# Optimization experiments

Measured on AMD Instinct MI355X. Metric: run time of the kernel, lower is better.

Reference implementation:

```python
import jax, jax.numpy as jnp
import numpy as np

DIST_THRESH = 0.5   # stands in for config.dist_thresh
ALPHA = 0.2         # LeakyReLU negative slope
NEG_INF = -9e15     # mask value used by the original module


def setup_inputs() -> dict:
    key = jax.random.key(0)
    k1, k2, k3 = jax.random.split(key, 3)
    N, dim = 8192, 128
    nodes = jax.random.normal(k1, (N, dim), dtype=jnp.float32)
    dist = jax.random.uniform(k2, (N, N), dtype=jnp.float32)
    # xavier_uniform on (2*dim, 1) with gain 1.414
    limit = 1.414 * np.sqrt(6.0 / (2 * dim + 1))
    a = jax.random.uniform(k3, (2 * dim, 1), dtype=jnp.float32,
                           minval=-limit, maxval=limit)
    return {"nodes": nodes, "dist": dist, "a": a}


def reference(nodes, dist, a):
    # Original math: e_ij = leakyrelu([h_i || h_j] @ a). Since a = [a1; a2],
    # this equals leakyrelu(h_i @ a1 + h_j @ a2) — same values, no N^2*2dim tensor.
    dim = nodes.shape[1]
    a1 = a[:dim, 0]                      # [dim]
    a2 = a[dim:, 0]                      # [dim]
    s1 = nodes @ a1                      # [N] — contribution of row node i
    s2 = nodes @ a2                      # [N] — contribution of col node j
    e = jax.nn.leaky_relu(s1[:, None] + s2[None, :], negative_slope=ALPHA)  # [N, N]
    masked = jnp.where(dist < DIST_THRESH, e, NEG_INF)
    attention = jax.nn.softmax(masked, axis=1)   # [N, N]
    h_prime = attention @ nodes                  # [N, dim]
    return h_prime
```

## Files before the change

kernel.cpp:

```cpp
#include <hip/hip_runtime.h>
#include <stdint.h>

#define NN 8192
#define DIM 128
#define ALPHA 0.2f
#define MTILE 32
#define BTHREADS 512
#define BK 256
#define NCHUNK (NN / BK)
#define WSTRIDE (BK + 8)

typedef float f32x16 __attribute__((ext_vector_type(16)));
typedef short bf16x8 __attribute__((ext_vector_type(8)));

__device__ __forceinline__ float b2f(uint32_t u){
  uint32_t x = u << 16;
  float f;
  __builtin_memcpy(&f, &x, 4);
  return f;
}
__device__ __forceinline__ uint16_t f2b(float f){
  uint32_t x;
  __builtin_memcpy(&x, &f, 4);
  x += 0x7FFFu + ((x >> 16) & 1u);
  return (uint16_t)(x >> 16);
}

__global__ void s_kernel(const float* __restrict__ nodes,
                         const float* __restrict__ a,
                         float* __restrict__ s1, float* __restrict__ s2){
  int row  = blockIdx.x * 4 + (threadIdx.x >> 6);
  int lane = threadIdx.x & 63;
  float2 nv  = *(const float2*)(nodes + row * DIM + lane * 2);
  float2 a1v = *(const float2*)(a + lane * 2);
  float2 a2v = *(const float2*)(a + DIM + lane * 2);
  float p1 = nv.x * a1v.x + nv.y * a1v.y;
  float p2 = nv.x * a2v.x + nv.y * a2v.y;
  #pragma unroll
  for (int off = 32; off; off >>= 1){
    p1 += __shfl_down(p1, off);
    p2 += __shfl_down(p2, off);
  }
  if (lane == 0){ s1[row] = p1; s2[row] = p2; }
}

__global__ void t_kernel(const float* __restrict__ nodes,
                         uint16_t* __restrict__ nodesT){
  __shared__ uint16_t tile[32][33];
  int kb = blockIdx.x * 32, nb = blockIdx.y * 32;
  int tx = threadIdx.x & 31, ty = threadIdx.x >> 5;
  for (int r = ty; r < 32; r += 8)
    tile[r][tx] = f2b(nodes[(size_t)(kb + r) * DIM + nb + tx]);
  __syncthreads();
  for (int r = ty; r < 32; r += 8)
    nodesT[(size_t)(nb + r) * NN + kb + tx] = tile[tx][r];
}

__global__ void __launch_bounds__(BTHREADS)
attn_kernel(const float* __restrict__ dist,
            const uint16_t* __restrict__ nodesT,
            const float* __restrict__ s1,
            const float* __restrict__ s2,
            float* __restrict__ out){
  __shared__ uint16_t Wbuf[2][MTILE][WSTRIDE];
  __shared__ float accT[MTILE][DIM];
  __shared__ float denT[MTILE];

  const int tid  = threadIdx.x;
  const int lane = tid & 63;
  const int wave = tid >> 6;
  const int i0   = blockIdx.x * MTILE;

  const int wrow = tid >> 4;
  const int wr   = tid & 15;
  const float s1v = s1[i0 + wrow];
  const float* distRow = dist + (size_t)(i0 + wrow) * NN + wr * 8;

  const int q    = wave & 3;
  const int h    = wave >> 2;
  const int m    = lane & 31;
  const int half = lane >> 5;
  const uint16_t* bRow = nodesT + (size_t)(q * 32 + m) * NN;

  f32x16 acc;
  #pragma unroll
  for (int i = 0; i < 16; i++) acc[i] = 0.f;
  float den = 0.f;

  float4 pd0, pd1, pd2, pd3, ps0, ps1, ps2, ps3;

  auto load_chunk = [&](int s){
    const float* dpp = distRow + s * BK;
    const float* spp = s2 + s * BK + wr * 8;
    pd0 = *(const float4*)(dpp);
    pd1 = *(const float4*)(dpp + 4);
    pd2 = *(const float4*)(dpp + 128);
    pd3 = *(const float4*)(dpp + 132);
    ps0 = *(const float4*)(spp);
    ps1 = *(const float4*)(spp + 4);
    ps2 = *(const float4*)(spp + 128);
    ps3 = *(const float4*)(spp + 132);
  };

  auto gen_write = [&](int buf){
    float dv[16] = {pd0.x, pd0.y, pd0.z, pd0.w, pd1.x, pd1.y, pd1.z, pd1.w,
                    pd2.x, pd2.y, pd2.z, pd2.w, pd3.x, pd3.y, pd3.z, pd3.w};
    float sv[16] = {ps0.x, ps0.y, ps0.z, ps0.w, ps1.x, ps1.y, ps1.z, ps1.w,
                    ps2.x, ps2.y, ps2.z, ps2.w, ps3.x, ps3.y, ps3.z, ps3.w};
    union { bf16x8 v; uint16_t u[8]; } w0, w1;
    #pragma unroll
    for (int j = 0; j < 8; j++){
      float x = s1v + sv[j];
      float e = fmaxf(x, ALPHA * x);
      float w = (dv[j] < 0.5f) ? __expf(e) : 0.f;
      uint16_t wq = f2b(w);
      w0.u[j] = wq;
      den += b2f((uint32_t)wq);
    }
    #pragma unroll
    for (int j = 0; j < 8; j++){
      float x = s1v + sv[8 + j];
      float e = fmaxf(x, ALPHA * x);
      float w = (dv[8 + j] < 0.5f) ? __expf(e) : 0.f;
      uint16_t wq = f2b(w);
      w1.u[j] = wq;
      den += b2f((uint32_t)wq);
    }
    *(bf16x8*)&Wbuf[buf][wrow][wr * 8]       = w0.v;
    *(bf16x8*)&Wbuf[buf][wrow][wr * 8 + 128] = w1.v;
  };

  load_chunk(0);
  gen_write(0);

  for (int s = 0; s < NCHUNK; s++){
    if (s + 1 < NCHUNK) load_chunk(s + 1);
    __syncthreads();
    const int buf = s & 1;
    const size_t kb = (size_t)s * BK;
    #pragma unroll
    for (int kk = 0; kk < 8; kk++){
      int ko = h * 128 + kk * 16 + half * 8;
      bf16x8 av = *(const bf16x8*)&Wbuf[buf][m][ko];
      bf16x8 bv = *(const bf16x8*)(bRow + kb + ko);
      acc = __builtin_amdgcn_mfma_f32_32x32x16_bf16(av, bv, acc, 0, 0, 0);
    }
    if (s + 1 < NCHUNK) gen_write((s + 1) & 1);
  }

  den += __shfl_down(den, 8, 16);
  den += __shfl_down(den, 4, 16);
  den += __shfl_down(den, 2, 16);
  den += __shfl_down(den, 1, 16);
  if (wr == 0) denT[wrow] = 1.0f / den;

  if (h == 0){
    #pragma unroll
    for (int r = 0; r < 16; r++){
      int row = (r & 3) + 8 * (r >> 2) + 4 * half;
      accT[row][q * 32 + m] = acc[r];
    }
  }
  __syncthreads();
  if (h == 1){
    #pragma unroll
    for (int r = 0; r < 16; r++){
      int row = (r & 3) + 8 * (r >> 2) + 4 * half;
      float v = (accT[row][q * 32 + m] + acc[r]) * denT[row];
      out[(size_t)(i0 + row) * DIM + q * 32 + m] = v;
    }
  }
}

extern "C" void kernel_launch(void* const* d_in, const int* in_sizes, int n_in,
                              void* d_out, int out_size, void* d_ws, size_t ws_size,
                              hipStream_t stream){
  const float* nodes = (const float*)d_in[0];
  const float* dist  = (const float*)d_in[1];
  const float* a     = (const float*)d_in[2];
  float* out = (float*)d_out;

  char* ws = (char*)d_ws;
  float*    s1     = (float*)ws;
  float*    s2     = (float*)(ws + (32 << 10));
  uint16_t* nodesT = (uint16_t*)(ws + (64 << 10));

  s_kernel<<<NN / 4, 256, 0, stream>>>(nodes, a, s1, s2);
  t_kernel<<<dim3(NN / 32, DIM / 32), 256, 0, stream>>>(nodes, nodesT);
  attn_kernel<<<NN / MTILE, BTHREADS, 0, stream>>>(dist, nodesT, s1, s2, out);
}
```

Baseline: 391.8 us.

## Halve row tile, switch to 16x16x32 MFMA, and fuse prep kernels

The attention kernel now processes 16 rows per block instead of 32. It uses 16x16x32 bf16 MFMAs, with each wave owning 16 output columns and the full K chunk, which removes the cross-wave LDS reduction. This gives twice as many blocks and lower LDS and register use (launch bounds ask for 4 blocks per CU), but each block reads the nodesT operand for half as many rows, so global B traffic doubles. The s-vector and transpose kernels are merged into one prep kernel that reads nodes once and writes the transposed bf16 copy with 16-byte stores, saving a launch.

```diff
diff --git a/kernel.cpp b/kernel.cpp
--- a/kernel.cpp
+++ b/kernel.cpp
@@ -4,13 +4,13 @@
 #define NN 8192
 #define DIM 128
 #define ALPHA 0.2f
-#define MTILE 32
+#define MTILE 16
 #define BTHREADS 512
 #define BK 256
 #define NCHUNK (NN / BK)
 #define WSTRIDE (BK + 8)
 
-typedef float f32x16 __attribute__((ext_vector_type(16)));
+typedef float f32x4 __attribute__((ext_vector_type(4)));
 typedef short bf16x8 __attribute__((ext_vector_type(8)));
 
 __device__ __forceinline__ float b2f(uint32_t u){
@@ -26,44 +26,71 @@
   return (uint16_t)(x >> 16);
 }
 
-__global__ void s_kernel(const float* __restrict__ nodes,
-                         const float* __restrict__ a,
-                         float* __restrict__ s1, float* __restrict__ s2){
-  int row  = blockIdx.x * 4 + (threadIdx.x >> 6);
-  int lane = threadIdx.x & 63;
-  float2 nv  = *(const float2*)(nodes + row * DIM + lane * 2);
-  float2 a1v = *(const float2*)(a + lane * 2);
-  float2 a2v = *(const float2*)(a + DIM + lane * 2);
-  float p1 = nv.x * a1v.x + nv.y * a1v.y;
-  float p2 = nv.x * a2v.x + nv.y * a2v.y;
+__global__ void __launch_bounds__(256)
+prep_kernel(const float* __restrict__ nodes, const float* __restrict__ a,
+            float* __restrict__ s1, float* __restrict__ s2,
+            uint16_t* __restrict__ nodesT){
+  __shared__ __align__(16) uint16_t tile[DIM][40];
+
+  const int r   = threadIdx.x >> 3;
+  const int t   = threadIdx.x & 7;
+  const int row = blockIdx.x * 32 + r;
+
+  const float* np = nodes + (size_t)row * DIM + t * 16;
+  float4 v0 = *(const float4*)(np);
+  float4 v1 = *(const float4*)(np + 4);
+  float4 v2 = *(const float4*)(np + 8);
+  float4 v3 = *(const float4*)(np + 12);
+
+  const float* a1p = a + t * 16;
+  const float* a2p = a + DIM + t * 16;
+  float4 b0 = *(const float4*)(a1p);
+  float4 b1 = *(const float4*)(a1p + 4);
+  float4 b2 = *(const float4*)(a1p + 8);
+  float4 b3 = *(const float4*)(a1p + 12);
+  float4 c0 = *(const float4*)(a2p);
+  float4 c1 = *(const float4*)(a2p + 4);
+  float4 c2 = *(const float4*)(a2p + 8);
+  float4 c3 = *(const float4*)(a2p + 12);
+
+  float p1 = v0.x*b0.x + v0.y*b0.y + v0.z*b0.z + v0.w*b0.w
+           + v1.x*b1.x + v1.y*b1.y + v1.z*b1.z + v1.w*b1.w
+           + v2.x*b2.x + v2.y*b2.y + v2.z*b2.z + v2.w*b2.w
+           + v3.x*b3.x + v3.y*b3.y + v3.z*b3.z + v3.w*b3.w;
+  float p2 = v0.x*c0.x + v0.y*c0.y + v0.z*c0.z + v0.w*c0.w
+           + v1.x*c1.x + v1.y*c1.y + v1.z*c1.z + v1.w*c1.w
+           + v2.x*c2.x + v2.y*c2.y + v2.z*c2.z + v2.w*c2.w
+           + v3.x*c3.x + v3.y*c3.y + v3.z*c3.z + v3.w*c3.w;
+
+  p1 += __shfl_down(p1, 4, 8);
+  p1 += __shfl_down(p1, 2, 8);
+  p1 += __shfl_down(p1, 1, 8);
+  p2 += __shfl_down(p2, 4, 8);
+  p2 += __shfl_down(p2, 2, 8);
+  p2 += __shfl_down(p2, 1, 8);
+  if (t == 0){ s1[row] = p1; s2[row] = p2; }
+
+  float vv[16] = {v0.x, v0.y, v0.z, v0.w, v1.x, v1.y, v1.z, v1.w,
+                  v2.x, v2.y, v2.z, v2.w, v3.x, v3.y, v3.z, v3.w};
   #pragma unroll
-  for (int off = 32; off; off >>= 1){
-    p1 += __shfl_down(p1, off);
-    p2 += __shfl_down(p2, off);
-  }
-  if (lane == 0){ s1[row] = p1; s2[row] = p2; }
+  for (int j = 0; j < 16; j++)
+    tile[t * 16 + j][r] = f2b(vv[j]);
+  __syncthreads();
+
+  const int n  = threadIdx.x >> 1;
+  const int hf = threadIdx.x & 1;
+  uint16_t* op = nodesT + (size_t)n * NN + blockIdx.x * 32 + hf * 16;
+  *(uint4*)(op)     = *(const uint4*)&tile[n][hf * 16];
+  *(uint4*)(op + 8) = *(const uint4*)&tile[n][hf * 16 + 8];
 }
 
-__global__ void t_kernel(const float* __restrict__ nodes,
-                         uint16_t* __restrict__ nodesT){
-  __shared__ uint16_t tile[32][33];
-  int kb = blockIdx.x * 32, nb = blockIdx.y * 32;
-  int tx = threadIdx.x & 31, ty = threadIdx.x >> 5;
-  for (int r = ty; r < 32; r += 8)
-    tile[r][tx] = f2b(nodes[(size_t)(kb + r) * DIM + nb + tx]);
-  __syncthreads();
-  for (int r = ty; r < 32; r += 8)
-    nodesT[(size_t)(nb + r) * NN + kb + tx] = tile[tx][r];
-}
-
-__global__ void __launch_bounds__(BTHREADS)
+__global__ void __launch_bounds__(BTHREADS, 4)
 attn_kernel(const float* __restrict__ dist,
             const uint16_t* __restrict__ nodesT,
             const float* __restrict__ s1,
             const float* __restrict__ s2,
             float* __restrict__ out){
-  __shared__ uint16_t Wbuf[2][MTILE][WSTRIDE];
-  __shared__ float accT[MTILE][DIM];
+  __shared__ __align__(16) uint16_t Wbuf[2][MTILE][WSTRIDE];
   __shared__ float denT[MTILE];
 
   const int tid  = threadIdx.x;
@@ -71,43 +98,33 @@
   const int wave = tid >> 6;
   const int i0   = blockIdx.x * MTILE;
 
-  const int wrow = tid >> 4;
-  const int wr   = tid & 15;
+  const int wrow = tid >> 5;
+  const int wr   = tid & 31;
   const float s1v = s1[i0 + wrow];
   const float* distRow = dist + (size_t)(i0 + wrow) * NN + wr * 8;
 
-  const int q    = wave & 3;
-  const int h    = wave >> 2;
-  const int m    = lane & 31;
-  const int half = lane >> 5;
-  const uint16_t* bRow = nodesT + (size_t)(q * 32 + m) * NN;
+  const int c = lane & 15;
+  const int g = lane >> 4;
+  const uint16_t* bRow = nodesT + (size_t)(wave * 16 + c) * NN + g * 8;
 
-  f32x16 acc;
-  #pragma unroll
-  for (int i = 0; i < 16; i++) acc[i] = 0.f;
+  f32x4 acc = {0.f, 0.f, 0.f, 0.f};
   float den = 0.f;
 
-  float4 pd0, pd1, pd2, pd3, ps0, ps1, ps2, ps3;
+  float4 pd0, pd1, ps0, ps1;
 
   auto load_chunk = [&](int s){
     const float* dpp = distRow + s * BK;
     const float* spp = s2 + s * BK + wr * 8;
     pd0 = *(const float4*)(dpp);
     pd1 = *(const float4*)(dpp + 4);
-    pd2 = *(const float4*)(dpp + 128);
-    pd3 = *(const float4*)(dpp + 132);
     ps0 = *(const float4*)(spp);
     ps1 = *(const float4*)(spp + 4);
-    ps2 = *(const float4*)(spp + 128);
-    ps3 = *(const float4*)(spp + 132);
   };
 
   auto gen_write = [&](int buf){
-    float dv[16] = {pd0.x, pd0.y, pd0.z, pd0.w, pd1.x, pd1.y, pd1.z, pd1.w,
-                    pd2.x, pd2.y, pd2.z, pd2.w, pd3.x, pd3.y, pd3.z, pd3.w};
-    float sv[16] = {ps0.x, ps0.y, ps0.z, ps0.w, ps1.x, ps1.y, ps1.z, ps1.w,
-                    ps2.x, ps2.y, ps2.z, ps2.w, ps3.x, ps3.y, ps3.z, ps3.w};
-    union { bf16x8 v; uint16_t u[8]; } w0, w1;
+    float dv[8] = {pd0.x, pd0.y, pd0.z, pd0.w, pd1.x, pd1.y, pd1.z, pd1.w};
+    float sv[8] = {ps0.x, ps0.y, ps0.z, ps0.w, ps1.x, ps1.y, ps1.z, ps1.w};
+    union { bf16x8 v; uint16_t u[8]; } w0;
     #pragma unroll
     for (int j = 0; j < 8; j++){
       float x = s1v + sv[j];
@@ -117,17 +134,7 @@
       w0.u[j] = wq;
       den += b2f((uint32_t)wq);
     }
-    #pragma unroll
-    for (int j = 0; j < 8; j++){
-      float x = s1v + sv[8 + j];
-      float e = fmaxf(x, ALPHA * x);
-      float w = (dv[8 + j] < 0.5f) ? __expf(e) : 0.f;
-      uint16_t wq = f2b(w);
-      w1.u[j] = wq;
-      den += b2f((uint32_t)wq);
-    }
-    *(bf16x8*)&Wbuf[buf][wrow][wr * 8]       = w0.v;
-    *(bf16x8*)&Wbuf[buf][wrow][wr * 8 + 128] = w1.v;
+    *(bf16x8*)&Wbuf[buf][wrow][wr * 8] = w0.v;
   };
 
   load_chunk(0);
@@ -140,35 +147,26 @@
     const size_t kb = (size_t)s * BK;
     #pragma unroll
     for (int kk = 0; kk < 8; kk++){
-      int ko = h * 128 + kk * 16 + half * 8;
-      bf16x8 av = *(const bf16x8*)&Wbuf[buf][m][ko];
+      const int ko = kk * 32;
+      bf16x8 av = *(const bf16x8*)&Wbuf[buf][c][ko + g * 8];
       bf16x8 bv = *(const bf16x8*)(bRow + kb + ko);
-      acc = __builtin_amdgcn_mfma_f32_32x32x16_bf16(av, bv, acc, 0, 0, 0);
+      acc = __builtin_amdgcn_mfma_f32_16x16x32_bf16(av, bv, acc, 0, 0, 0);
     }
     if (s + 1 < NCHUNK) gen_write((s + 1) & 1);
   }
 
-  den += __shfl_down(den, 8, 16);
-  den += __shfl_down(den, 4, 16);
-  den += __shfl_down(den, 2, 16);
-  den += __shfl_down(den, 1, 16);
+  den += __shfl_down(den, 16, 32);
+  den += __shfl_down(den, 8, 32);
+  den += __shfl_down(den, 4, 32);
+  den += __shfl_down(den, 2, 32);
+  den += __shfl_down(den, 1, 32);
   if (wr == 0) denT[wrow] = 1.0f / den;
+  __syncthreads();
 
-  if (h == 0){
-    #pragma unroll
-    for (int r = 0; r < 16; r++){
-      int row = (r & 3) + 8 * (r >> 2) + 4 * half;
-      accT[row][q * 32 + m] = acc[r];
-    }
-  }
-  __syncthreads();
-  if (h == 1){
-    #pragma unroll
-    for (int r = 0; r < 16; r++){
-      int row = (r & 3) + 8 * (r >> 2) + 4 * half;
-      float v = (accT[row][q * 32 + m] + acc[r]) * denT[row];
-      out[(size_t)(i0 + row) * DIM + q * 32 + m] = v;
-    }
+  #pragma unroll
+  for (int r = 0; r < 4; r++){
+    const int row = g * 4 + r;
+    out[(size_t)(i0 + row) * DIM + wave * 16 + c] = acc[r] * denT[row];
   }
 }
 
@@ -185,7 +183,6 @@
   float*    s2     = (float*)(ws + (32 << 10));
   uint16_t* nodesT = (uint16_t*)(ws + (64 << 10));
 
-  s_kernel<<<NN / 4, 256, 0, stream>>>(nodes, a, s1, s2);
-  t_kernel<<<dim3(NN / 32, DIM / 32), 256, 0, stream>>>(nodes, nodesT);
+  prep_kernel<<<NN / 32, 256, 0, stream>>>(nodes, a, s1, s2, nodesT);
   attn_kernel<<<NN / MTILE, BTHREADS, 0, stream>>>(dist, nodesT, s1, s2, out);
 }
```

Result: slower. 447.0 us (+14.1%).

## Use single-wave blocks with register-resident weights and 16x16x32 MFMA

Applied to the files above, without the earlier changes.

Each block is now one wave that handles 16 rows. It computes the bf16 attention weights straight into the MFMA A-operand registers, so the LDS staging buffer and block barriers are gone, and it prefetches dist/s2 four stages ahead. This removes LDS traffic and synchronisation. In exchange, each wave reloads the nodesT B-operand from global memory for every 16-row tile, so nodesT traffic doubles relative to the 32-row tiles, and the grid grows to 512 tiny blocks.

```diff
diff --git a/kernel.cpp b/kernel.cpp
--- a/kernel.cpp
+++ b/kernel.cpp
@@ -4,13 +4,10 @@
 #define NN 8192
 #define DIM 128
 #define ALPHA 0.2f
-#define MTILE 32
-#define BTHREADS 512
-#define BK 256
-#define NCHUNK (NN / BK)
-#define WSTRIDE (BK + 8)
+#define NK (NN / 32)
+#define PF 4
 
-typedef float f32x16 __attribute__((ext_vector_type(16)));
+typedef float f32x4 __attribute__((ext_vector_type(4)));
 typedef short bf16x8 __attribute__((ext_vector_type(8)));
 
 __device__ __forceinline__ float b2f(uint32_t u){
@@ -56,120 +53,91 @@
     nodesT[(size_t)(nb + r) * NN + kb + tx] = tile[tx][r];
 }
 
-__global__ void __launch_bounds__(BTHREADS)
+__global__ void __launch_bounds__(64)
 attn_kernel(const float* __restrict__ dist,
             const uint16_t* __restrict__ nodesT,
             const float* __restrict__ s1,
             const float* __restrict__ s2,
             float* __restrict__ out){
-  __shared__ uint16_t Wbuf[2][MTILE][WSTRIDE];
-  __shared__ float accT[MTILE][DIM];
-  __shared__ float denT[MTILE];
+  const int lane = threadIdx.x;
+  const int c    = lane & 15;
+  const int g    = lane >> 4;
+  const int i0   = blockIdx.x * 16;
 
-  const int tid  = threadIdx.x;
-  const int lane = tid & 63;
-  const int wave = tid >> 6;
-  const int i0   = blockIdx.x * MTILE;
+  const float  s1v  = s1[i0 + c];
+  const float* dptr = dist + (size_t)(i0 + c) * NN + g * 8;
+  const float* sptr = s2 + g * 8;
 
-  const int wrow = tid >> 4;
-  const int wr   = tid & 15;
-  const float s1v = s1[i0 + wrow];
-  const float* distRow = dist + (size_t)(i0 + wrow) * NN + wr * 8;
-
-  const int q    = wave & 3;
-  const int h    = wave >> 2;
-  const int m    = lane & 31;
-  const int half = lane >> 5;
-  const uint16_t* bRow = nodesT + (size_t)(q * 32 + m) * NN;
-
-  f32x16 acc;
+  f32x4 acc[8];
   #pragma unroll
-  for (int i = 0; i < 16; i++) acc[i] = 0.f;
+  for (int d = 0; d < 8; d++) acc[d] = (f32x4){0.f, 0.f, 0.f, 0.f};
   float den = 0.f;
 
-  float4 pd0, pd1, pd2, pd3, ps0, ps1, ps2, ps3;
+  float4 pd0[PF], pd1[PF], ps0[PF], ps1[PF];
+  #pragma unroll
+  for (int p = 0; p < PF; p++){
+    pd0[p] = *(const float4*)(dptr + p * 32);
+    pd1[p] = *(const float4*)(dptr + p * 32 + 4);
+    ps0[p] = *(const float4*)(sptr + p * 32);
+    ps1[p] = *(const float4*)(sptr + p * 32 + 4);
+  }
 
-  auto load_chunk = [&](int s){
-    const float* dpp = distRow + s * BK;
-    const float* spp = s2 + s * BK + wr * 8;
-    pd0 = *(const float4*)(dpp);
-    pd1 = *(const float4*)(dpp + 4);
-    pd2 = *(const float4*)(dpp + 128);
-    pd3 = *(const float4*)(dpp + 132);
-    ps0 = *(const float4*)(spp);
-    ps1 = *(const float4*)(spp + 4);
-    ps2 = *(const float4*)(spp + 128);
-    ps3 = *(const float4*)(spp + 132);
-  };
+  auto stage = [&](int p, int kk, bool prefetch){
+    bf16x8 bv[8];
+    #pragma unroll
+    for (int d = 0; d < 8; d++)
+      bv[d] = *(const bf16x8*)(nodesT + (size_t)(d * 16 + c) * NN + kk * 32 + g * 8);
 
-  auto gen_write = [&](int buf){
-    float dv[16] = {pd0.x, pd0.y, pd0.z, pd0.w, pd1.x, pd1.y, pd1.z, pd1.w,
-                    pd2.x, pd2.y, pd2.z, pd2.w, pd3.x, pd3.y, pd3.z, pd3.w};
-    float sv[16] = {ps0.x, ps0.y, ps0.z, ps0.w, ps1.x, ps1.y, ps1.z, ps1.w,
-                    ps2.x, ps2.y, ps2.z, ps2.w, ps3.x, ps3.y, ps3.z, ps3.w};
-    union { bf16x8 v; uint16_t u[8]; } w0, w1;
+    float dv[8] = {pd0[p].x, pd0[p].y, pd0[p].z, pd0[p].w,
+                   pd1[p].x, pd1[p].y, pd1[p].z, pd1[p].w};
+    float sv[8] = {ps0[p].x, ps0[p].y, ps0[p].z, ps0[p].w,
+                   ps1[p].x, ps1[p].y, ps1[p].z, ps1[p].w};
+    union { bf16x8 v; uint16_t u[8]; } w;
     #pragma unroll
     for (int j = 0; j < 8; j++){
       float x = s1v + sv[j];
       float e = fmaxf(x, ALPHA * x);
-      float w = (dv[j] < 0.5f) ? __expf(e) : 0.f;
-      uint16_t wq = f2b(w);
-      w0.u[j] = wq;
+      float wf = (dv[j] < 0.5f) ? __expf(e) : 0.f;
+      uint16_t wq = f2b(wf);
+      w.u[j] = wq;
       den += b2f((uint32_t)wq);
     }
+
+    if (prefetch){
+      const int kn = kk + PF;
+      pd0[p] = *(const float4*)(dptr + kn * 32);
+      pd1[p] = *(const float4*)(dptr + kn * 32 + 4);
+      ps0[p] = *(const float4*)(sptr + kn * 32);
+      ps1[p] = *(const float4*)(sptr + kn * 32 + 4);
+    }
+
     #pragma unroll
-    for (int j = 0; j < 8; j++){
-      float x = s1v + sv[8 + j];
-      float e = fmaxf(x, ALPHA * x);
-      float w = (dv[8 + j] < 0.5f) ? __expf(e) : 0.f;
-      uint16_t wq = f2b(w);
-      w1.u[j] = wq;
-      den += b2f((uint32_t)wq);
-    }
-    *(bf16x8*)&Wbuf[buf][wrow][wr * 8]       = w0.v;
-    *(bf16x8*)&Wbuf[buf][wrow][wr * 8 + 128] = w1.v;
+    for (int d = 0; d < 8; d++)
+      acc[d] = __builtin_amdgcn_mfma_f32_16x16x32_bf16(w.v, bv[d], acc[d], 0, 0, 0);
   };
 
-  load_chunk(0);
-  gen_write(0);
+  for (int kko = 0; kko < NK - PF; kko += PF){
+    #pragma unroll
+    for (int p = 0; p < PF; p++)
+      stage(p, kko + p, true);
+  }
+  #pragma unroll
+  for (int p = 0; p < PF; p++)
+    stage(p, NK - PF + p, false);
 
-  for (int s = 0; s < NCHUNK; s++){
-    if (s + 1 < NCHUNK) load_chunk(s + 1);
-    __syncthreads();
-    const int buf = s & 1;
-    const size_t kb = (size_t)s * BK;
+  den += __shfl_down(den, 32);
+  den += __shfl_down(den, 16);
+
+  float inv[4];
+  #pragma unroll
+  for (int r = 0; r < 4; r++)
+    inv[r] = 1.0f / __shfl(den, g * 4 + r);
+
+  #pragma unroll
+  for (int d = 0; d < 8; d++)
     #pragma unroll
-    for (int kk = 0; kk < 8; kk++){
-      int ko = h * 128 + kk * 16 + half * 8;
-      bf16x8 av = *(const bf16x8*)&Wbuf[buf][m][ko];
-      bf16x8 bv = *(const bf16x8*)(bRow + kb + ko);
-      acc = __builtin_amdgcn_mfma_f32_32x32x16_bf16(av, bv, acc, 0, 0, 0);
-    }
-    if (s + 1 < NCHUNK) gen_write((s + 1) & 1);
-  }
-
-  den += __shfl_down(den, 8, 16);
-  den += __shfl_down(den, 4, 16);
-  den += __shfl_down(den, 2, 16);
-  den += __shfl_down(den, 1, 16);
-  if (wr == 0) denT[wrow] = 1.0f / den;
-
-  if (h == 0){
-    #pragma unroll
-    for (int r = 0; r < 16; r++){
-      int row = (r & 3) + 8 * (r >> 2) + 4 * half;
-      accT[row][q * 32 + m] = acc[r];
-    }
-  }
-  __syncthreads();
-  if (h == 1){
-    #pragma unroll
-    for (int r = 0; r < 16; r++){
-      int row = (r & 3) + 8 * (r >> 2) + 4 * half;
-      float v = (accT[row][q * 32 + m] + acc[r]) * denT[row];
-      out[(size_t)(i0 + row) * DIM + q * 32 + m] = v;
-    }
-  }
+    for (int r = 0; r < 4; r++)
+      out[(size_t)(i0 + g * 4 + r) * DIM + d * 16 + c] = acc[d][r] * inv[r];
 }
 
 extern "C" void kernel_launch(void* const* d_in, const int* in_sizes, int n_in,
@@ -187,5 +155,5 @@
 
   s_kernel<<<NN / 4, 256, 0, stream>>>(nodes, a, s1, s2);
   t_kernel<<<dim3(NN / 32, DIM / 32), 256, 0, stream>>>(nodes, nodesT);
-  attn_kernel<<<NN / MTILE, BTHREADS, 0, stream>>>(dist, nodesT, s1, s2, out);
+  attn_kernel<<<NN / 16, 64, 0, stream>>>(dist, nodesT, s1, s2, out);
 }
```

Result: slower. 577.1 us (+47.3%).

## Deepen dist prefetch to two chunks and use lightweight LDS-only barrier

Applied to the files above, without the earlier changes.

Unrolls the main loop by two with two register sets, so each chunk's dist/s2 loads are issued two iterations before use instead of one. The block barrier now waits only on LDS counters (lgkmcnt), so in-flight global loads can stay outstanding across it. The nodesT B-operand loads are also hoisted ahead of the MFMA chain. The goal is to hide HBM latency on the dist stream, at the cost of more registers, which could lower occupancy.

```diff
diff --git a/kernel.cpp b/kernel.cpp
--- a/kernel.cpp
+++ b/kernel.cpp
@@ -24,6 +24,12 @@
   __builtin_memcpy(&x, &f, 4);
   x += 0x7FFFu + ((x >> 16) & 1u);
   return (uint16_t)(x >> 16);
+}
+
+__device__ __forceinline__ void bar_lds(){
+  asm volatile("s_waitcnt lgkmcnt(0)" ::: "memory");
+  __builtin_amdgcn_s_barrier();
+  asm volatile("" ::: "memory");
 }
 
 __global__ void s_kernel(const float* __restrict__ nodes,
@@ -87,65 +93,77 @@
   for (int i = 0; i < 16; i++) acc[i] = 0.f;
   float den = 0.f;
 
-  float4 pd0, pd1, pd2, pd3, ps0, ps1, ps2, ps3;
-
-  auto load_chunk = [&](int s){
-    const float* dpp = distRow + s * BK;
-    const float* spp = s2 + s * BK + wr * 8;
-    pd0 = *(const float4*)(dpp);
-    pd1 = *(const float4*)(dpp + 4);
-    pd2 = *(const float4*)(dpp + 128);
-    pd3 = *(const float4*)(dpp + 132);
-    ps0 = *(const float4*)(spp);
-    ps1 = *(const float4*)(spp + 4);
-    ps2 = *(const float4*)(spp + 128);
-    ps3 = *(const float4*)(spp + 132);
-  };
-
-  auto gen_write = [&](int buf){
-    float dv[16] = {pd0.x, pd0.y, pd0.z, pd0.w, pd1.x, pd1.y, pd1.z, pd1.w,
-                    pd2.x, pd2.y, pd2.z, pd2.w, pd3.x, pd3.y, pd3.z, pd3.w};
-    float sv[16] = {ps0.x, ps0.y, ps0.z, ps0.w, ps1.x, ps1.y, ps1.z, ps1.w,
-                    ps2.x, ps2.y, ps2.z, ps2.w, ps3.x, ps3.y, ps3.z, ps3.w};
-    union { bf16x8 v; uint16_t u[8]; } w0, w1;
-    #pragma unroll
-    for (int j = 0; j < 8; j++){
-      float x = s1v + sv[j];
-      float e = fmaxf(x, ALPHA * x);
-      float w = (dv[j] < 0.5f) ? __expf(e) : 0.f;
-      uint16_t wq = f2b(w);
-      w0.u[j] = wq;
-      den += b2f((uint32_t)wq);
-    }
-    #pragma unroll
-    for (int j = 0; j < 8; j++){
-      float x = s1v + sv[8 + j];
-      float e = fmaxf(x, ALPHA * x);
-      float w = (dv[8 + j] < 0.5f) ? __expf(e) : 0.f;
-      uint16_t wq = f2b(w);
-      w1.u[j] = wq;
-      den += b2f((uint32_t)wq);
-    }
-    *(bf16x8*)&Wbuf[buf][wrow][wr * 8]       = w0.v;
-    *(bf16x8*)&Wbuf[buf][wrow][wr * 8 + 128] = w1.v;
-  };
-
-  load_chunk(0);
-  gen_write(0);
-
-  for (int s = 0; s < NCHUNK; s++){
-    if (s + 1 < NCHUNK) load_chunk(s + 1);
-    __syncthreads();
-    const int buf = s & 1;
-    const size_t kb = (size_t)s * BK;
-    #pragma unroll
-    for (int kk = 0; kk < 8; kk++){
-      int ko = h * 128 + kk * 16 + half * 8;
-      bf16x8 av = *(const bf16x8*)&Wbuf[buf][m][ko];
-      bf16x8 bv = *(const bf16x8*)(bRow + kb + ko);
-      acc = __builtin_amdgcn_mfma_f32_32x32x16_bf16(av, bv, acc, 0, 0, 0);
-    }
-    if (s + 1 < NCHUNK) gen_write((s + 1) & 1);
+  float4 Ad0, Ad1, Ad2, Ad3, As0, As1, As2, As3;
+  float4 Bd0, Bd1, Bd2, Bd3, Bs0, Bs1, Bs2, Bs3;
+
+#define LOADC(d0,d1,d2,d3,e0,e1,e2,e3, s_) do{                         \
+    const float* dpp = distRow + (size_t)(s_) * BK;                    \
+    const float* spp = s2 + (s_) * BK + wr * 8;                        \
+    d0 = *(const float4*)(dpp);        d1 = *(const float4*)(dpp + 4); \
+    d2 = *(const float4*)(dpp + 128);  d3 = *(const float4*)(dpp + 132);\
+    e0 = *(const float4*)(spp);        e1 = *(const float4*)(spp + 4); \
+    e2 = *(const float4*)(spp + 128);  e3 = *(const float4*)(spp + 132);\
+  }while(0)
+
+#define GENW(d0,d1,d2,d3,e0,e1,e2,e3, buf_) do{                        \
+    float dv[16] = {d0.x,d0.y,d0.z,d0.w, d1.x,d1.y,d1.z,d1.w,          \
+                    d2.x,d2.y,d2.z,d2.w, d3.x,d3.y,d3.z,d3.w};         \
+    float sv[16] = {e0.x,e0.y,e0.z,e0.w, e1.x,e1.y,e1.z,e1.w,          \
+                    e2.x,e2.y,e2.z,e2.w, e3.x,e3.y,e3.z,e3.w};         \
+    union { bf16x8 v; uint16_t u[8]; } w0, w1;                         \
+    _Pragma("unroll")                                                  \
+    for (int j = 0; j < 8; j++){                                       \
+      float x = s1v + sv[j];                                           \
+      float e = fmaxf(x, ALPHA * x);                                   \
+      float w = (dv[j] < 0.5f) ? __expf(e) : 0.f;                      \
+      uint16_t wq = f2b(w);                                            \
+      w0.u[j] = wq;                                                    \
+      den += b2f((uint32_t)wq);                                        \
+    }                                                                  \
+    _Pragma("unroll")                                                  \
+    for (int j = 0; j < 8; j++){                                       \
+      float x = s1v + sv[8 + j];                                       \
+      float e = fmaxf(x, ALPHA * x);                                   \
+      float w = (dv[8 + j] < 0.5f) ? __expf(e) : 0.f;                  \
+      uint16_t wq = f2b(w);                                            \
+      w1.u[j] = wq;                                                    \
+      den += b2f((uint32_t)wq);                                        \
+    }                                                                  \
+    *(bf16x8*)&Wbuf[buf_][wrow][wr * 8]       = w0.v;                  \
+    *(bf16x8*)&Wbuf[buf_][wrow][wr * 8 + 128] = w1.v;                  \
+  }while(0)
+
+#define MFMAC(buf_, s_) do{                                            \
+    const size_t kb = (size_t)(s_) * BK;                               \
+    bf16x8 bvv[8];                                                     \
+    _Pragma("unroll")                                                  \
+    for (int kk = 0; kk < 8; kk++)                                     \
+      bvv[kk] = *(const bf16x8*)(bRow + kb + h * 128 + kk * 16 + half * 8);\
+    _Pragma("unroll")                                                  \
+    for (int kk = 0; kk < 8; kk++){                                    \
+      int ko = h * 128 + kk * 16 + half * 8;                           \
+      bf16x8 av = *(const bf16x8*)&Wbuf[buf_][m][ko];                  \
+      acc = __builtin_amdgcn_mfma_f32_32x32x16_bf16(av, bvv[kk], acc, 0, 0, 0);\
+    }                                                                  \
+  }while(0)
+
+  LOADC(Ad0,Ad1,Ad2,Ad3,As0,As1,As2,As3, 0);
+  GENW (Ad0,Ad1,Ad2,Ad3,As0,As1,As2,As3, 0);
+  LOADC(Bd0,Bd1,Bd2,Bd3,Bs0,Bs1,Bs2,Bs3, 1);
+
+  for (int s = 0; s < NCHUNK; s += 2){
+    bar_lds();
+    if (s + 2 < NCHUNK)
+      LOADC(Ad0,Ad1,Ad2,Ad3,As0,As1,As2,As3, s + 2);
+    MFMAC(0, s);
+    GENW (Bd0,Bd1,Bd2,Bd3,Bs0,Bs1,Bs2,Bs3, 1);
+
+    bar_lds();
+    if (s + 3 < NCHUNK)
+      LOADC(Bd0,Bd1,Bd2,Bd3,Bs0,Bs1,Bs2,Bs3, s + 3);
+    MFMAC(1, s + 1);
+    if (s + 2 < NCHUNK)
+      GENW (Ad0,Ad1,Ad2,Ad3,As0,As1,As2,As3, 0);
   }
 
   den += __shfl_down(den, 8, 16);
```

Measured after the change: 397.6 us. No clear change (+1.5%).
